# Kernel optimization log

Hardware: AMD Instinct MI355X
Metric: run time of the kernel (lower is better)

Reference implementation:

```python
import jax, jax.numpy as jnp
import numpy as np

N, E, G = 50000, 320000, 256
BN_EPS = 1e-5
HEADS = 4


def _bn(x, g, b):
    # eval-mode BatchNorm1d with running_mean=0, running_var=1
    return g * (x * np.float32(1.0 / np.sqrt(1.0 + BN_EPS))) + b


def _mlp(x, w1, b1, w2, b2):
    return jax.nn.relu(x @ w1 + b1) @ w2 + b2


def _gatv2(x, src, dst, ea, lw, lb, rw, rb, ew, att, bias):
    n = x.shape[0]
    H = HEADS
    C = lw.shape[1] // H
    # self-loops with edge_attr = mean of incoming edge features (fill_value='mean')
    deg = jax.ops.segment_sum(jnp.ones((ea.shape[0],), x.dtype), dst, num_segments=n)
    loop_ea = jax.ops.segment_sum(ea, dst, num_segments=n) / jnp.maximum(deg, 1.0)[:, None]
    ar = jnp.arange(n)
    s = jnp.concatenate([src, ar])
    d = jnp.concatenate([dst, ar])
    ea_all = jnp.concatenate([ea, loop_ea], axis=0)
    xl = (x @ lw + lb).reshape(n, H, C)   # lin_l (source / message features)
    xr = (x @ rw + rb).reshape(n, H, C)   # lin_r (target)
    ee = (ea_all @ ew).reshape(-1, H, C)  # lin_edge (no bias)
    m = jax.nn.leaky_relu(xl[s] + xr[d] + ee, 0.2)       # [E+N, H, C]
    a = jnp.einsum('ehc,hc->eh', m, att)                 # attention logits
    amax = jax.ops.segment_max(a, d, num_segments=n)
    ex = jnp.exp(a - amax[d])
    den = jax.ops.segment_sum(ex, d, num_segments=n)
    w = ex / den[d]                                      # scatter-softmax over target
    out = jax.ops.segment_sum(xl[s] * w[..., None], d, num_segments=n)
    return out.reshape(n, H * C) + bias


def _meta(x, ea, u, src, dst, batch, ep, gp, up):
    # EdgeModel -> NodeModel(GATv2 + relu) -> GlobalModel (residuals=False, eval dropout)
    ea2 = _mlp(jnp.concatenate([x[src], x[dst], ea], axis=1), *ep)
    xn = jax.nn.relu(_gatv2(x, src, dst, ea2, *gp))
    pooled = jax.ops.segment_sum(xn, batch, num_segments=G)
    u2 = _mlp(jnp.concatenate([u, pooled], axis=1), *up)
    return xn, ea2, u2


def _forward(x, edge_attr, e1_w1, e1_b1, e1_w2, e1_b2, g1_lw, g1_lb, g1_rw, g1_rb, g1_ew, g1_att, g1_bias, u1_w1, u1_b1, u1_w2, u1_b2, bn_n_g, bn_n_b, bn_e_g, bn_e_b, bn_u_g, bn_u_b, e2_w1, e2_b1, e2_w2, e2_b2, g2_lw, g2_lb, g2_rw, g2_rb, g2_ew, g2_att, g2_bias, u2_w1, u2_b1, u2_w2, u2_b2, fc1_w, fc1_b, fc2_w, fc2_b, src, dst, batch):
    u0 = jnp.zeros((G, 256), x.dtype)
    x1, ea1, u1 = _meta(x, edge_attr, u0, src, dst, batch,
                        (e1_w1, e1_b1, e1_w2, e1_b2),
                        (g1_lw, g1_lb, g1_rw, g1_rb, g1_ew, g1_att, g1_bias),
                        (u1_w1, u1_b1, u1_w2, u1_b2))
    x1 = _bn(x1, bn_n_g, bn_n_b)
    ea1 = _bn(ea1, bn_e_g, bn_e_b)
    u1 = _bn(u1, bn_u_g, bn_u_b)
    _, _, u2 = _meta(x1, ea1, u1, src, dst, batch,
                     (e2_w1, e2_b1, e2_w2, e2_b2),
                     (g2_lw, g2_lb, g2_rw, g2_rb, g2_ew, g2_att, g2_bias),
                     (u2_w1, u2_b1, u2_w2, u2_b2))
    h = jax.nn.relu(u2 @ fc1_w + fc1_b)
    return h @ fc2_w + fc2_b


def setup_inputs() -> dict:
    key = jax.random.key(0)
    ks = iter(jax.random.split(key, 64))
    rp = lambda shape: jax.random.normal(next(ks), shape, jnp.float32) * 0.05
    inp = {}
    inp['x'] = jax.random.normal(next(ks), (N, 64), jnp.float32)
    inp['edge_attr'] = jax.random.normal(next(ks), (E, 16), jnp.float32)
    # layer 1: EdgeModel(64,16,h=64,out=128), GATv2(64->256,H=4,edge=128), Global(256+256->256)
    inp.update(e1_w1=rp((144, 64)), e1_b1=rp((64,)), e1_w2=rp((64, 128)), e1_b2=rp((128,)))
    inp.update(g1_lw=rp((64, 256)), g1_lb=rp((256,)), g1_rw=rp((64, 256)), g1_rb=rp((256,)),
               g1_ew=rp((128, 256)), g1_att=rp((4, 64)), g1_bias=rp((256,)))
    inp.update(u1_w1=rp((512, 256)), u1_b1=rp((256,)), u1_w2=rp((256, 256)), u1_b2=rp((256,)))
    inp.update(bn_n_g=jnp.ones((256,), jnp.float32), bn_n_b=jnp.zeros((256,), jnp.float32),
               bn_e_g=jnp.ones((128,), jnp.float32), bn_e_b=jnp.zeros((128,), jnp.float32),
               bn_u_g=jnp.ones((256,), jnp.float32), bn_u_b=jnp.zeros((256,), jnp.float32))
    # layer 2: EdgeModel(256,128,h=128,out=128), GATv2(256->256,H=4,edge=128), Global
    inp.update(e2_w1=rp((640, 128)), e2_b1=rp((128,)), e2_w2=rp((128, 128)), e2_b2=rp((128,)))
    inp.update(g2_lw=rp((256, 256)), g2_lb=rp((256,)), g2_rw=rp((256, 256)), g2_rb=rp((256,)),
               g2_ew=rp((128, 256)), g2_att=rp((4, 64)), g2_bias=rp((256,)))
    inp.update(u2_w1=rp((512, 256)), u2_b1=rp((256,)), u2_w2=rp((256, 256)), u2_b2=rp((256,)))
    inp.update(fc1_w=rp((256, 64)), fc1_b=rp((64,)), fc2_w=rp((64, 1)), fc2_b=rp((1,)))
    inp['edge_index'] = jax.random.randint(next(ks), (2, E), 0, N, jnp.int64)
    inp['batch'] = jnp.sort(jax.random.randint(next(ks), (N,), 0, G, jnp.int64))
    return inp


def reference(x, edge_attr, e1_w1, e1_b1, e1_w2, e1_b2, g1_lw, g1_lb, g1_rw, g1_rb, g1_ew, g1_att, g1_bias, u1_w1, u1_b1, u1_w2, u1_b2, bn_n_g, bn_n_b, bn_e_g, bn_e_b, bn_u_g, bn_u_b, e2_w1, e2_b1, e2_w2, e2_b2, g2_lw, g2_lb, g2_rw, g2_rb, g2_ew, g2_att, g2_bias, u2_w1, u2_b1, u2_w2, u2_b2, fc1_w, fc1_b, fc2_w, fc2_b, edge_index, batch):
    return _forward(x, edge_attr, e1_w1, e1_b1, e1_w2, e1_b2, g1_lw, g1_lb, g1_rw, g1_rb, g1_ew, g1_att, g1_bias, u1_w1, u1_b1, u1_w2, u1_b2, bn_n_g, bn_n_b, bn_e_g, bn_e_b, bn_u_g, bn_u_b, e2_w1, e2_b1, e2_w2, e2_b2, g2_lw, g2_lb, g2_rw, g2_rb, g2_ew, g2_att, g2_bias, u2_w1, u2_b1, u2_w2, u2_b2, fc1_w, fc1_b, fc2_w, fc2_b, edge_index[0], edge_index[1], batch)
```

## Files before the change

### kernel.cpp

```cpp
#include <hip/hip_runtime.h>
#include <hip/hip_bf16.h>
#include <hip/hip_fp8.h>
#include <cstdint>
#include <cstddef>

#define INVS 0.99999500003749968f
#define G_GRAPHS 256

using bf16 = __hip_bfloat16;
using short8 = __attribute__((ext_vector_type(8))) short;
using floatx4 = __attribute__((ext_vector_type(4))) float;

__device__ __forceinline__ unsigned short f2bf(float v) {
    union { float f; unsigned u; } x; x.f = v;
    unsigned r = x.u + 0x7fffu + ((x.u >> 16) & 1u);
    return (unsigned short)(r >> 16);
}
__device__ __forceinline__ float bfu(unsigned short u) { return __uint_as_float((unsigned)u << 16); }
__device__ __forceinline__ float bfu_lo(unsigned v) { return __uint_as_float(v << 16); }
__device__ __forceinline__ float bfu_hi(unsigned v) { return __uint_as_float(v & 0xffff0000u); }
__device__ __forceinline__ float fp82f(unsigned char b) {
    __hip_fp8_e4m3 q; q.__x = b; return (float)q;
}
__device__ __forceinline__ unsigned pk_bf16(float a, float b) {
// ... 192 lines not shown
    for (int tt = 0; tt < 2; ++tt) {
        int col = (nq + tt) * 16 + lr;
        float bv = (col >= 64) ? b1[col - 64] : 0.f;
        for (int r = 0; r < 4; ++r)
            Ot[lq * 4 + r][col] = (short)f2bf(acc[tt][r] + bv);
    }
    __syncthreads();
    {
        int r = t >> 4, c = t & 15;
        long long n = n0 + r;
        if (n < N)
            *(short8*)(void*)(pre1 + n * 128 + c * 8) = *(const short8*)&Ot[r][c * 8];
    }
}

__global__ __launch_bounds__(256) void edge_mlp1_mfma_k(
    const bf16* __restrict__ pre1, const float* __restrict__ ea,
    const int* __restrict__ csr_src, const int* __restrict__ csr_dst,
    const int* __restrict__ csr_eid,
    const short* __restrict__ w1c,
    const short* __restrict__ w2s, const float* __restrict__ b2,
    const short* __restrict__ ews,
    unsigned char* __restrict__ ee8, int NT, int E) {
    __shared__ float Ps[32][76];
    __shared__ short Ae[32][40];
    __shared__ short Ht[32][72];
    __shared__ short A2[32][136];
    __shared__ int sdv[32][3];
    unsigned char* Et = (unsigned char*)&Ps[0][0];
    int t = threadIdx.x;
    long long s0 = (long long)blockIdx.x * 32;
    if (t < 96) {
        int r = t & 31, which = t >> 5;
        long long s = s0 + r;
        int v = (which == 2) ? E : 0;
        if (s < NT) v = (which == 0) ? csr_src[s] : (which == 1 ? csr_dst[s] : csr_eid[s]);
        sdv[r][which] = v;
    }
    __syncthreads();
    {
        int r = t >> 3, c = t & 7;
        long long s = s0 + r;
        bool ok = (s < NT) && (sdv[r][2] < E);
        float p[8];
        if (ok) {
            short8 vs = *(const short8*)(const void*)(pre1 + (long long)sdv[r][0] * 128 + c * 8);
// ... 92 lines not shown
        for (int tt = 0; tt < 8; ++tt) {
            int ch0 = (mb + tt) * 16 + lq * 4;
            unsigned u = pk_fp8x4(acc3[tt][0], acc3[tt][1], acc3[tt][2], acc3[tt][3]);
            *(unsigned*)(Et + sl * 272 + ch0) = u;
        }
    }
    __syncthreads();
    for (int i = t; i < 512; i += 256) {
        int r = i >> 4, c = i & 15;
        long long s = s0 + r;
        if (s < NT)
            *(uint4*)(ee8 + s * 256 + c * 16) = *(const uint4*)(Et + r * 272 + c * 16);
    }
}

template <int K, typename T>
__global__ __launch_bounds__(256) void node_linear_mfma_k(
    const T* x, const short* __restrict__ ws,
    const float* __restrict__ bl, const float* __restrict__ br,
    bf16* __restrict__ xl, bf16* xr, int N) {
    __shared__ short At[16][K + 8];
    __shared__ short Ot[16][520];
    int t = threadIdx.x;
    long long n0 = (long long)blockIdx.x * 16;
    if (sizeof(T) == 4) {
        for (int i = t; i < 16 * (K / 4); i += 256) {
            int r = i / (K / 4), c = i % (K / 4);
            long long n = n0 + r;
            float4 v = {0.f, 0.f, 0.f, 0.f};
            if (n < N) v = *(const float4*)((const float*)x + n * K + c * 4);
            ushort4 pk;
            pk.x = f2bf(v.x); pk.y = f2bf(v.y); pk.z = f2bf(v.z); pk.w = f2bf(v.w);
            *(ushort4*)&At[r][c * 4] = pk;
        }
    } else {
        for (int i = t; i < 16 * (K / 8); i += 256) {
            int r = i / (K / 8), c = i % (K / 8);
            long long n = n0 + r;
            short8 v = {0, 0, 0, 0, 0, 0, 0, 0};
            if (n < N) v = *(const short8*)(const void*)((const bf16*)x + n * K + c * 8);
            *(short8*)&At[r][c * 8] = v;
        }
    }
    __syncthreads();

    int w = t >> 6, lane = t & 63;
    int nr = lane & 15, lq = lane >> 4;

    floatx4 acc[8];
    #pragma unroll
    for (int i = 0; i < 8; ++i) acc[i] = (floatx4){0.f, 0.f, 0.f, 0.f};
    for (int kk = 0; kk < K / 32; ++kk) {
        short8 bfr = *(const short8*)&At[nr][kk * 32 + lq * 8];
        #pragma unroll
        for (int tt = 0; tt < 8; ++tt) {
            short8 a = *(const short8*)(ws + ((long long)((kk * 32 + w * 8 + tt) * 64 + lane)) * 8);
            acc[tt] = __builtin_amdgcn_mfma_f32_16x16x32_bf16(a, bfr, acc[tt], 0, 0, 0);
        }
    }
    #pragma unroll
    for (int tt = 0; tt < 8; ++tt) {
        int ch0 = (w * 8 + tt) * 16 + lq * 4;
        const float* bp = (ch0 < 256) ? (bl + ch0) : (br + (ch0 - 256));
        float4 bv = *(const float4*)bp;
        uint2 o;
        o.x = pk_bf16(acc[tt][0] + bv.x, acc[tt][1] + bv.y);
        o.y = pk_bf16(acc[tt][2] + bv.z, acc[tt][3] + bv.w);
        *(uint2*)&Ot[nr][ch0] = o;
    }
    __syncthreads();
    for (int i = t; i < 1024; i += 256) {
        int r = i >> 6, c = i & 63;
        long long n = n0 + r;
        if (n < N) {
            short8 v = *(const short8*)&Ot[r][c * 8];
            if (c < 32) *(short8*)(void*)(xl + n * 256 + c * 8) = v;
            else        *(short8*)(void*)(xr + n * 256 + (c - 32) * 8) = v;
        }
    }
}

__global__ __launch_bounds__(256) void pre_mfma_k(
    const bf16* __restrict__ x, const short* __restrict__ ws,
    const float* __restrict__ bx, bf16* __restrict__ out, int N) {
    __shared__ short At[16][264];
    __shared__ short Ot[16][264];
    int t = threadIdx.x;
    long long n0 = (long long)blockIdx.x * 16;
    for (int i = t; i < 512; i += 256) {
        int r = i >> 5, c = i & 31;
        long long n = n0 + r;
        short8 v = {0, 0, 0, 0, 0, 0, 0, 0};
        if (n < N) v = *(const short8*)(const void*)(x + n * 256 + c * 8);
        *(short8*)&At[r][c * 8] = v;
    }
    __syncthreads();
// ... 15 lines not shown
    #pragma unroll
    for (int tt = 0; tt < 4; ++tt) {
        int ch0 = (w * 4 + tt) * 16 + lq * 4;
        float4 bv = *(const float4*)(bx + ch0);
        uint2 o;
        o.x = pk_bf16(acc[tt][0] + bv.x, acc[tt][1] + bv.y);
        o.y = pk_bf16(acc[tt][2] + bv.z, acc[tt][3] + bv.w);
        *(uint2*)&Ot[nr][ch0] = o;
    }
    __syncthreads();
    for (int i = t; i < 512; i += 256) {
        int r = i >> 5, c = i & 31;
        long long n = n0 + r;
        if (n < N)
            *(short8*)(void*)(out + n * 256 + c * 8) = *(const short8*)&Ot[r][c * 8];
    }
}

template <bool L1>
__global__ __launch_bounds__(256) void gat_fused_k(
    const unsigned char* __restrict__ ee8, const bf16* __restrict__ xl, const bf16* xr,
    const int* __restrict__ off, const int* __restrict__ csr_src,
    const float* __restrict__ att, const float* __restrict__ bias,
    const float* __restrict__ bng, const float* __restrict__ bnb,
    const int* __restrict__ batch,
    bf16* x1bn, float* __restrict__ pooled, int N) {
    __shared__ float ps[4][260];
    __shared__ int bid[4];
    int t = threadIdx.x;
    int w = t >> 6, lane = t & 63;
// ... 154 lines not shown
        int f = g2 >> 6, lane = g2 & 63;
        int kk = f >> 3, tt = f & 7;
        int n = tt * 16 + (lane & 15);
        int k0 = kk * 32 + (lane >> 4) * 8;
        short8 v;
        for (int j = 0; j < 8; ++j) v[j] = (short)f2bf(w2[(k0 + j) * 128 + n]);
        *(short8*)(w2s + (long long)g2 * 8) = v;
    } else if (gid < 12544) {
        int j = gid - 12288;
        b1x[j] = 0.f;
    } else if (gid < 12672) {
        int j = gid - 12544;
        float acc = b1[j];
        for (int c = 0; c < 128; ++c) acc += bb[c] * w1[(512 + c) * 128 + j];
        b1x[128 + j] = acc;
    }
}

__global__ __launch_bounds__(256) void edge_mlp2_mfma_k(
    const bf16* __restrict__ xpre, const bf16* __restrict__ pre1,
    const float* __restrict__ ea,
    const int* __restrict__ csr_src, const int* __restrict__ csr_dst,
    const int* __restrict__ csr_eid,
    const short* __restrict__ w1c, const short* __restrict__ w2s1,
    const float* __restrict__ e1_b2,
    const short* __restrict__ w1s,
    const short* __restrict__ w2s, const float* __restrict__ b2,
    const short* __restrict__ ews,
    unsigned char* __restrict__ ee8, int NT, int E) {
    __shared__ short Zt[32][136];
    __shared__ short Ht[32][136];
    __shared__ short Xt[32][136];
    __shared__ int sdv[32][3];
    unsigned char* Et = (unsigned char*)&Xt[0][0];
    int t = threadIdx.x;
    long long s0 = (long long)blockIdx.x * 32;
    if (t < 96) {
        int r = t & 31, which = t >> 5;
        long long s = s0 + r;
        int v = (which == 2) ? E : 0;
        if (s < NT) v = (which == 0) ? csr_src[s] : (which == 1 ? csr_dst[s] : csr_eid[s]);
        sdv[r][which] = v;
    }
    __syncthreads();
    {
        int r = t >> 3, c = t & 7;
        long long s = s0 + r;
        bool ok = (s < NT) && (sdv[r][2] < E);
        uint4 o = {0, 0, 0, 0};
        if (ok) {
            short8 vs = *(const short8*)(const void*)(pre1 + (long long)sdv[r][0] * 128 + c * 8);
            short8 vd = *(const short8*)(const void*)(pre1 + (long long)sdv[r][1] * 128 + 64 + c * 8);
            float p[8];
            #pragma unroll
            for (int j = 0; j < 8; ++j)
                p[j] = bfu((unsigned short)vs[j]) + bfu((unsigned short)vd[j]);
            o.x = pk_bf16(p[0], p[1]); o.y = pk_bf16(p[2], p[3]);
            o.z = pk_bf16(p[4], p[5]); o.w = pk_bf16(p[6], p[7]);
        }
        *(uint4*)&Zt[r][c * 8] = o;
    }
    if (t < 128) {
        int r = t >> 2, c = t & 3;
        long long s = s0 + r;
        int eid = sdv[r][2];
        float4 v = {0.f, 0.f, 0.f, 0.f};
        if (s < NT && eid < E) v = *(const float4*)(ea + (long long)eid * 16 + c * 4);
        ushort4 pk;
        pk.x = f2bf(v.x); pk.y = f2bf(v.y); pk.z = f2bf(v.z); pk.w = f2bf(v.w);
        *(ushort4*)&Zt[r][96 + c * 4] = pk;
    } else {
        int i = t - 128;
        int r = i >> 2, c = i & 3;
        *(ushort4*)&Zt[r][96 + 16 + c * 4] = (ushort4){0, 0, 0, 0};
    }
    __syncthreads();

    int w = t >> 6, lane = t & 63;
    int sl = (w & 1) * 16 + (lane & 15);
    int lq = lane >> 4;

    {
        int mb = (w >> 1) * 2;
        floatx4 acc[2];
        #pragma unroll
        for (int tt = 0; tt < 2; ++tt) {
            uint2 pv = *(const uint2*)&Zt[sl][(mb + tt) * 16 + lq * 4];
            acc[tt] = (floatx4){bfu_lo(pv.x), bfu_hi(pv.x), bfu_lo(pv.y), bfu_hi(pv.y)};
        }
        short8 bfr = *(const short8*)&Zt[sl][96 + lq * 8];
        #pragma unroll
        for (int tt = 0; tt < 2; ++tt) {
            short8 a = *(const short8*)(w1c + ((long long)((mb + tt) * 64 + lane)) * 8);
            acc[tt] = __builtin_amdgcn_mfma_f32_16x16x32_bf16(a, bfr, acc[tt], 0, 0, 0);
        }
        #pragma unroll
        for (int tt = 0; tt < 2; ++tt) {
            int ch0 = (mb + tt) * 16 + lq * 4;
            uint2 o;
            o.x = pk_bf16(fmaxf(acc[tt][0], 0.f), fmaxf(acc[tt][1], 0.f));
            o.y = pk_bf16(fmaxf(acc[tt][2], 0.f), fmaxf(acc[tt][3], 0.f));
            *(uint2*)&Ht[sl][ch0] = o;
        }
    }
    __syncthreads();

    for (int i = t; i < 512; i += 256) {
        int r = i >> 4, c = i & 15;
        long long s = s0 + r;
        bool ok = (s < NT) && (sdv[r][2] < E);
        uint4 o = {0, 0, 0, 0};
        if (ok) {
            short8 vs = *(const short8*)(const void*)(xpre + (long long)sdv[r][0] * 256 + c * 8);
            short8 vd = *(const short8*)(const void*)(xpre + (long long)sdv[r][1] * 256 + 128 + c * 8);
            float p[8];
            #pragma unroll
            for (int j = 0; j < 8; ++j)
                p[j] = bfu((unsigned short)vs[j]) + bfu((unsigned short)vd[j]);
            o.x = pk_bf16(p[0], p[1]); o.y = pk_bf16(p[2], p[3]);
            o.z = pk_bf16(p[4], p[5]); o.w = pk_bf16(p[6], p[7]);
        }
        *(uint4*)&Xt[r][c * 8] = o;
    }
    {
        int mb = (w >> 1) * 4;
        floatx4 acc2[4];
        #pragma unroll
        for (int i = 0; i < 4; ++i) acc2[i] = (floatx4){0.f, 0.f, 0.f, 0.f};
        #pragma unroll
        for (int kk = 0; kk < 2; ++kk) {
            short8 bfr = *(const short8*)&Ht[sl][kk * 32 + lq * 8];
            #pragma unroll
            for (int tt = 0; tt < 4; ++tt) {
                short8 a = *(const short8*)(w2s1 + ((long long)((kk * 8 + mb + tt) * 64 + lane)) * 8);
                acc2[tt] = __builtin_amdgcn_mfma_f32_16x16x32_bf16(a, bfr, acc2[tt], 0, 0, 0);
            }
        }
        #pragma unroll
        for (int tt = 0; tt < 4; ++tt) {
            int ch0 = (mb + tt) * 16 + lq * 4;
            float4 bv = *(const float4*)(e1_b2 + ch0);
            uint2 o;
            o.x = pk_bf16(acc2[tt][0] + bv.x, acc2[tt][1] + bv.y);
            o.y = pk_bf16(acc2[tt][2] + bv.z, acc2[tt][3] + bv.w);
            *(uint2*)&Zt[sl][ch0] = o;
        }
    }
    __syncthreads();

    {
        int mb = (w >> 1) * 4;
        floatx4 acc[4];
        #pragma unroll
        for (int tt = 0; tt < 4; ++tt) {
            uint2 pv = *(const uint2*)&Xt[sl][(mb + tt) * 16 + lq * 4];
            acc[tt] = (floatx4){bfu_lo(pv.x), bfu_hi(pv.x), bfu_lo(pv.y), bfu_hi(pv.y)};
        }
        #pragma unroll
        for (int kk = 0; kk < 4; ++kk) {
            short8 bfr = *(const short8*)&Zt[sl][kk * 32 + lq * 8];
            #pragma unroll
            for (int tt = 0; tt < 4; ++tt) {
                short8 a = *(const short8*)(w1s + ((long long)(((16 + kk) * 8 + mb + tt) * 64 + lane)) * 8);
                acc[tt] = __builtin_amdgcn_mfma_f32_16x16x32_bf16(a, bfr, acc[tt], 0, 0, 0);
            }
        }
        #pragma unroll
        for (int tt = 0; tt < 4; ++tt) {
            int ch0 = (mb + tt) * 16 + lq * 4;
            uint2 o;
            o.x = pk_bf16(fmaxf(acc[tt][0], 0.f), fmaxf(acc[tt][1], 0.f));
            o.y = pk_bf16(fmaxf(acc[tt][2], 0.f), fmaxf(acc[tt][3], 0.f));
            *(uint2*)&Ht[sl][ch0] = o;
        }
    }
    __syncthreads();

    {
        int mb = (w >> 1) * 4;
        floatx4 acc2[4];
        #pragma unroll
        for (int i = 0; i < 4; ++i) acc2[i] = (floatx4){0.f, 0.f, 0.f, 0.f};
        #pragma unroll
        for (int kk = 0; kk < 4; ++kk) {
            short8 bfr = *(const short8*)&Ht[sl][kk * 32 + lq * 8];
            #pragma unroll
            for (int tt = 0; tt < 4; ++tt) {
                short8 a = *(const short8*)(w2s + ((long long)((kk * 8 + mb + tt) * 64 + lane)) * 8);
                acc2[tt] = __builtin_amdgcn_mfma_f32_16x16x32_bf16(a, bfr, acc2[tt], 0, 0, 0);
            }
        }
        #pragma unroll
        for (int tt = 0; tt < 4; ++tt) {
            int ch0 = (mb + tt) * 16 + lq * 4;
            float4 bv = *(const float4*)(b2 + ch0);
            uint2 o;
            o.x = pk_bf16(acc2[tt][0] + bv.x, acc2[tt][1] + bv.y);
            o.y = pk_bf16(acc2[tt][2] + bv.z, acc2[tt][3] + bv.w);
            *(uint2*)&Zt[sl][ch0] = o;
        }
    }
    __syncthreads();

    {
        int mb = (w >> 1) * 8;
        floatx4 acc3[8];
        #pragma unroll
        for (int i = 0; i < 8; ++i) acc3[i] = (floatx4){0.f, 0.f, 0.f, 0.f};
        #pragma unroll
        for (int kk = 0; kk < 4; ++kk) {
            short8 bfr = *(const short8*)&Zt[sl][kk * 32 + lq * 8];
            #pragma unroll
            for (int tt = 0; tt < 8; ++tt) {
                short8 a = *(const short8*)(ews + ((long long)((kk * 16 + mb + tt) * 64 + lane)) * 8);
                acc3[tt] = __builtin_amdgcn_mfma_f32_16x16x32_bf16(a, bfr, acc3[tt], 0, 0, 0);
            }
        }
        #pragma unroll
        for (int tt = 0; tt < 8; ++tt) {
            int ch0 = (mb + tt) * 16 + lq * 4;
            unsigned u = pk_fp8x4(acc3[tt][0], acc3[tt][1], acc3[tt][2], acc3[tt][3]);
            *(unsigned*)(Et + sl * 272 + ch0) = u;
        }
    }
    __syncthreads();
    for (int i = t; i < 512; i += 256) {
        int r = i >> 4, c = i & 15;
        long long s = s0 + r;
        if (s < NT && sdv[r][2] < E)
            *(uint4*)(ee8 + s * 256 + c * 16) = *(const uint4*)(Et + r * 272 + c * 16);
    }
}

__global__ void final_mlp_k(const float* __restrict__ u1bn, const float* __restrict__ pooled,
                            const float* __restrict__ w1, const float* __restrict__ b1,
                            const float* __restrict__ w2, const float* __restrict__ b2,
                            const float* __restrict__ f1w, const float* __restrict__ f1b,
                            const float* __restrict__ f2w, const float* __restrict__ f2b,
                            float* __restrict__ out) {
    __shared__ float ub[256], pb[256], h[256], u2[256];
    int t = threadIdx.x, g = blockIdx.x;
    ub[t] = u1bn[g * 256 + t];
    pb[t] = pooled[g * 256 + t];
    __syncthreads();
    float acc = b1[t];
// ... 58 lines not shown
    const float* u2_b2 = (const float*)d_in[37];
    const float* fc1_w = (const float*)d_in[38];
    const float* fc1_b = (const float*)d_in[39];
    const float* fc2_w = (const float*)d_in[40];
    const float* fc2_b = (const float*)d_in[41];
    const int* edge_index = (const int*)d_in[42];
    const int* batch = (const int*)d_in[43];

    const int N = in_sizes[0] / 64;
    const int E = in_sizes[1] / 16;
    const int NT = E + N;
    const int G = G_GRAPHS;
    const int* src = edge_index;
    const int* dst = edge_index + E;
    const int NB = (NT + 31) / 32;
    const int NSB = (N + 2047) / 2048;

    char* p = (char*)d_ws;
    auto alloc = [&](size_t bytes) { char* r = p; p += (bytes + 255) & ~(size_t)255; return r; };
    bf16* xl    = (bf16*)alloc((size_t)N * 256 * 2);
    bf16* xr    = (bf16*)alloc((size_t)N * 256 * 2);
    bf16* x1bn  = xr;
    unsigned char* ee8 = (unsigned char*)alloc((size_t)NT * 256);
    bf16* pre1  = (bf16*)alloc((size_t)N * 128 * 2);
    int* degi   = (int*)alloc((size_t)N * 4);
    int* off    = (int*)alloc((size_t)(N + 1) * 4);
    int* fillc  = (int*)alloc((size_t)N * 4);
    int* csr_src = (int*)alloc((size_t)NT * 4);
    int* csr_dst = (int*)alloc((size_t)NT * 4);
    int* csr_eid = (int*)alloc((size_t)NT * 4);
    int* bsum   = (int*)alloc((size_t)(NSB + 1) * 4);
    int* boff   = (int*)alloc((size_t)(NSB + 1) * 4);
    float* pooled = (float*)alloc((size_t)G * 256 * 4);
    float* u1bn = (float*)alloc((size_t)G * 256 * 4);
    short* w1s  = (short*)alloc((size_t)20 * 8 * 64 * 8 * 2);
    short* w2s  = (short*)alloc((size_t)4 * 8 * 64 * 8 * 2);
    float* b1x  = (float*)alloc((size_t)256 * 4);
// ... 11 lines not shown
    hipMemsetAsync(pooled, 0, (size_t)G * 256 * 4, stream);
    degi_k<<<(E + 255) / 256, 256, 0, stream>>>(dst, degi, E);
    scan_blk_k<<<NSB, 1024, 0, stream>>>(degi, off, bsum, N);
    scan_top_k<<<1, 64, 0, stream>>>(bsum, boff, off, NSB, N);
    scan_add_k<<<(N + 255) / 256, 256, 0, stream>>>(off, boff, N);
    fill_csr_k<<<(max(E, N) + 255) / 256, 256, 0, stream>>>(src, dst, off, fillc,
                                                            csr_src, csr_dst, csr_eid, E, N);

    conv_weights1_k<<<9, 256, 0, stream>>>(e1_w1, e1_w2, w1p, w1c, w2s1);
    conv_ew_k<<<16, 256, 0, stream>>>(g1_ew, ews1);
    conv_ew_k<<<16, 256, 0, stream>>>(g2_ew, ews2);
    conv_nodew_k<64><<<16, 256, 0, stream>>>(g1_lw, g1_rw, nw1);
    conv_nodew_k<256><<<64, 256, 0, stream>>>(g2_lw, g2_rw, nw2);
    conv_pre2w_k<<<32, 256, 0, stream>>>(e2_w1, nwp);
    pre1_mfma_k<<<(N + 15) / 16, 256, 0, stream>>>(x, w1p, e1_b1, pre1, N);
    edge_mlp1_mfma_k<<<NB, 256, 0, stream>>>(pre1, edge_attr, csr_src, csr_dst, csr_eid,
                                             w1c, w2s1, e1_b2, ews1, ee8, NT, E);
    node_linear_mfma_k<64, float><<<(N + 15) / 16, 256, 0, stream>>>(x, nw1, g1_lb, g1_rb, xl, xr, N);
    gat_fused_k<true><<<(N + 3) / 4, 256, 0, stream>>>(ee8, xl, xr, off, csr_src,
                                                       g1_att, g1_bias, bn_n_g, bn_n_b,
                                                       batch, x1bn, pooled, N);
    global_mlp1_k<<<G, 256, 0, stream>>>(pooled, u1_w1, u1_b1, u1_w2, u1_b2, bn_u_g, bn_u_b, u1bn);

    conv_weights_k<<<50, 256, 0, stream>>>(e2_w1, e2_w2, e2_b1, bn_e_g, bn_e_b, w1s, w2s, b1x);
    pre_mfma_k<<<(N + 15) / 16, 256, 0, stream>>>(x1bn, nwp, b1x, xl, N);
    edge_mlp2_mfma_k<<<NB, 256, 0, stream>>>(xl, pre1, edge_attr, csr_src, csr_dst, csr_eid,
                                             w1c, w2s1, e1_b2, w1s, w2s, e2_b2, ews2,
                                             ee8, NT, E);
    node_linear_mfma_k<256, bf16><<<(N + 15) / 16, 256, 0, stream>>>(x1bn, nw2, g2_lb, g2_rb, xl, xr, N);
    hipMemsetAsync(pooled, 0, (size_t)G * 256 * 4, stream);
    gat_fused_k<false><<<(N + 3) / 4, 256, 0, stream>>>(ee8, xl, xr, off, csr_src,
                                                        g2_att, g2_bias, nullptr, nullptr,
                                                        batch, nullptr, pooled, N);
    final_mlp_k<<<G, 256, 0, stream>>>(u1bn, pooled, u2_w1, u2_b1, u2_w2, u2_b2,
                                       fc1_w, fc1_b, fc2_w, fc2_b, (float*)d_out);
}
```

Measured before the change: 695.4 us.

## Merge node-linear GEMMs into edge-MLP kernels as extra blocks of one launch

The node lin_l/lin_r projection and the edge MLP now run as one kernel launch per layer. The first NLB blocks do the node projection and the remaining blocks do the edge MLP, with both paths sharing one raw shared-memory buffer. Layer 2 gets separate xl2/xr2 buffers so the node projection no longer overwrites xl, which the edge MLP still reads as its precomputed input. This removes a launch and its serialization and lets the two independent workloads overlap on the GPU. In exchange it costs extra workspace memory, and the shared-memory size is set by the larger path, which may lower occupancy.

```diff
diff --git a/kernel.cpp b/kernel.cpp
--- a/kernel.cpp
+++ b/kernel.cpp
@@ -230,7 +230,10 @@
     }
 }
 
-__global__ __launch_bounds__(256) void edge_mlp1_mfma_k(
+__global__ __launch_bounds__(256) void fused_l1_k(
+    const float* __restrict__ x, const short* __restrict__ nw,
+    const float* __restrict__ bl, const float* __restrict__ br,
+    bf16* __restrict__ xl, bf16* __restrict__ xr, int N, int NLB,
     const bf16* __restrict__ pre1, const float* __restrict__ ea,
     const int* __restrict__ csr_src, const int* __restrict__ csr_dst,
     const int* __restrict__ csr_eid,
@@ -238,14 +241,64 @@
     const short* __restrict__ w2s, const float* __restrict__ b2,
     const short* __restrict__ ews,
     unsigned char* __restrict__ ee8, int NT, int E) {
-    __shared__ float Ps[32][76];
-    __shared__ short Ae[32][40];
-    __shared__ short Ht[32][72];
-    __shared__ short A2[32][136];
-    __shared__ int sdv[32][3];
-    unsigned char* Et = (unsigned char*)&Ps[0][0];
+    __shared__ __align__(16) char smem[25984];
     int t = threadIdx.x;
-    long long s0 = (long long)blockIdx.x * 32;
+    if ((int)blockIdx.x < NLB) {
+        short (*At)[72]  = (short(*)[72])smem;
+        short (*Ot)[520] = (short(*)[520])(smem + 2304);
+        long long n0 = (long long)blockIdx.x * 16;
+        {
+            int r = t >> 4, c = t & 15;
+            long long n = n0 + r;
+            float4 v = {0.f, 0.f, 0.f, 0.f};
+            if (n < N) v = *(const float4*)(x + n * 64 + c * 4);
+            ushort4 pk;
+            pk.x = f2bf(v.x); pk.y = f2bf(v.y); pk.z = f2bf(v.z); pk.w = f2bf(v.w);
+            *(ushort4*)&At[r][c * 4] = pk;
+        }
+        __syncthreads();
+        int w = t >> 6, lane = t & 63;
+        int nr = lane & 15, lq = lane >> 4;
+        floatx4 acc[8];
+        #pragma unroll
+        for (int i = 0; i < 8; ++i) acc[i] = (floatx4){0.f, 0.f, 0.f, 0.f};
+        for (int kk = 0; kk < 2; ++kk) {
+            short8 bfr = *(const short8*)&At[nr][kk * 32 + lq * 8];
+            #pragma unroll
+            for (int tt = 0; tt < 8; ++tt) {
+                short8 a = *(const short8*)(nw + ((long long)((kk * 32 + w * 8 + tt) * 64 + lane)) * 8);
+                acc[tt] = __builtin_amdgcn_mfma_f32_16x16x32_bf16(a, bfr, acc[tt], 0, 0, 0);
+            }
+        }
+        #pragma unroll
+        for (int tt = 0; tt < 8; ++tt) {
+            int ch0 = (w * 8 + tt) * 16 + lq * 4;
+            const float* bp = (ch0 < 256) ? (bl + ch0) : (br + (ch0 - 256));
+            float4 bv = *(const float4*)bp;
+            uint2 o;
+            o.x = pk_bf16(acc[tt][0] + bv.x, acc[tt][1] + bv.y);
+            o.y = pk_bf16(acc[tt][2] + bv.z, acc[tt][3] + bv.w);
+            *(uint2*)&Ot[nr][ch0] = o;
+        }
+        __syncthreads();
+        for (int i = t; i < 1024; i += 256) {
+            int r = i >> 6, c = i & 63;
+            long long n = n0 + r;
+            if (n < N) {
+                short8 v = *(const short8*)&Ot[r][c * 8];
+                if (c < 32) *(short8*)(void*)(xl + n * 256 + c * 8) = v;
+                else        *(short8*)(void*)(xr + n * 256 + (c - 32) * 8) = v;
+            }
+        }
+        return;
+    }
+    float (*Ps)[76]  = (float(*)[76])smem;
+    short (*Ae)[40]  = (short(*)[40])(smem + 9728);
+    short (*Ht)[72]  = (short(*)[72])(smem + 12288);
+    short (*A2)[136] = (short(*)[136])(smem + 16896);
+    int (*sdv)[3]    = (int(*)[3])(smem + 25600);
+    unsigned char* Et = (unsigned char*)smem;
+    long long s0 = (long long)(blockIdx.x - NLB) * 32;
     if (t < 96) {
         int r = t & 31, which = t >> 5;
         long long s = s0 + r;
@@ -368,72 +421,6 @@
     }
 }
 
-template <int K, typename T>
-__global__ __launch_bounds__(256) void node_linear_mfma_k(
-    const T* x, const short* __restrict__ ws,
-    const float* __restrict__ bl, const float* __restrict__ br,
-    bf16* __restrict__ xl, bf16* xr, int N) {
-    __shared__ short At[16][K + 8];
-    __shared__ short Ot[16][520];
-    int t = threadIdx.x;
-    long long n0 = (long long)blockIdx.x * 16;
-    if (sizeof(T) == 4) {
-        for (int i = t; i < 16 * (K / 4); i += 256) {
-            int r = i / (K / 4), c = i % (K / 4);
-            long long n = n0 + r;
-            float4 v = {0.f, 0.f, 0.f, 0.f};
-            if (n < N) v = *(const float4*)((const float*)x + n * K + c * 4);
-            ushort4 pk;
-            pk.x = f2bf(v.x); pk.y = f2bf(v.y); pk.z = f2bf(v.z); pk.w = f2bf(v.w);
-            *(ushort4*)&At[r][c * 4] = pk;
-        }
-    } else {
-        for (int i = t; i < 16 * (K / 8); i += 256) {
-            int r = i / (K / 8), c = i % (K / 8);
-            long long n = n0 + r;
-            short8 v = {0, 0, 0, 0, 0, 0, 0, 0};
-            if (n < N) v = *(const short8*)(const void*)((const bf16*)x + n * K + c * 8);
-            *(short8*)&At[r][c * 8] = v;
-        }
-    }
-    __syncthreads();
-
-    int w = t >> 6, lane = t & 63;
-    int nr = lane & 15, lq = lane >> 4;
-
-    floatx4 acc[8];
-    #pragma unroll
-    for (int i = 0; i < 8; ++i) acc[i] = (floatx4){0.f, 0.f, 0.f, 0.f};
-    for (int kk = 0; kk < K / 32; ++kk) {
-        short8 bfr = *(const short8*)&At[nr][kk * 32 + lq * 8];
-        #pragma unroll
-        for (int tt = 0; tt < 8; ++tt) {
-            short8 a = *(const short8*)(ws + ((long long)((kk * 32 + w * 8 + tt) * 64 + lane)) * 8);
-            acc[tt] = __builtin_amdgcn_mfma_f32_16x16x32_bf16(a, bfr, acc[tt], 0, 0, 0);
-        }
-    }
-    #pragma unroll
-    for (int tt = 0; tt < 8; ++tt) {
-        int ch0 = (w * 8 + tt) * 16 + lq * 4;
-        const float* bp = (ch0 < 256) ? (bl + ch0) : (br + (ch0 - 256));
-        float4 bv = *(const float4*)bp;
-        uint2 o;
-        o.x = pk_bf16(acc[tt][0] + bv.x, acc[tt][1] + bv.y);
-        o.y = pk_bf16(acc[tt][2] + bv.z, acc[tt][3] + bv.w);
-        *(uint2*)&Ot[nr][ch0] = o;
-    }
-    __syncthreads();
-    for (int i = t; i < 1024; i += 256) {
-        int r = i >> 6, c = i & 63;
-        long long n = n0 + r;
-        if (n < N) {
-            short8 v = *(const short8*)&Ot[r][c * 8];
-            if (c < 32) *(short8*)(void*)(xl + n * 256 + c * 8) = v;
-            else        *(short8*)(void*)(xr + n * 256 + (c - 32) * 8) = v;
-        }
-    }
-}
-
 __global__ __launch_bounds__(256) void pre_mfma_k(
     const bf16* __restrict__ x, const short* __restrict__ ws,
     const float* __restrict__ bx, bf16* __restrict__ out, int N) {
@@ -479,6 +466,272 @@
         long long n = n0 + r;
         if (n < N)
             *(short8*)(void*)(out + n * 256 + c * 8) = *(const short8*)&Ot[r][c * 8];
+    }
+}
+
+__global__ __launch_bounds__(256) void fused_l2_k(
+    const bf16* __restrict__ xin, const short* __restrict__ nw,
+    const float* __restrict__ bl, const float* __restrict__ br,
+    bf16* __restrict__ xl2, bf16* __restrict__ xr2, int N, int NLB,
+    const bf16* __restrict__ xpre, const bf16* __restrict__ pre1,
+    const float* __restrict__ ea,
+    const int* __restrict__ csr_src, const int* __restrict__ csr_dst,
+    const int* __restrict__ csr_eid,
+    const short* __restrict__ w1c, const short* __restrict__ w2s1,
+    const float* __restrict__ e1_b2,
+    const short* __restrict__ w1s,
+    const short* __restrict__ w2s, const float* __restrict__ b2,
+    const short* __restrict__ ews,
+    unsigned char* __restrict__ ee8, int NT, int E) {
+    __shared__ __align__(16) char smem[26496];
+    int t = threadIdx.x;
+    if ((int)blockIdx.x < NLB) {
+        short (*At)[264] = (short(*)[264])smem;
+        short (*Ot)[520] = (short(*)[520])(smem + 8448);
+        long long n0 = (long long)blockIdx.x * 16;
+        for (int i = t; i < 512; i += 256) {
+            int r = i >> 5, c = i & 31;
+            long long n = n0 + r;
+            short8 v = {0, 0, 0, 0, 0, 0, 0, 0};
+            if (n < N) v = *(const short8*)(const void*)(xin + n * 256 + c * 8);
+            *(short8*)&At[r][c * 8] = v;
+        }
+        __syncthreads();
+        int w = t >> 6, lane = t & 63;
+        int nr = lane & 15, lq = lane >> 4;
+        floatx4 acc[8];
+        #pragma unroll
+        for (int i = 0; i < 8; ++i) acc[i] = (floatx4){0.f, 0.f, 0.f, 0.f};
+        for (int kk = 0; kk < 8; ++kk) {
+            short8 bfr = *(const short8*)&At[nr][kk * 32 + lq * 8];
+            #pragma unroll
+            for (int tt = 0; tt < 8; ++tt) {
+                short8 a = *(const short8*)(nw + ((long long)((kk * 32 + w * 8 + tt) * 64 + lane)) * 8);
+                acc[tt] = __builtin_amdgcn_mfma_f32_16x16x32_bf16(a, bfr, acc[tt], 0, 0, 0);
+            }
+        }
+        #pragma unroll
+        for (int tt = 0; tt < 8; ++tt) {
+            int ch0 = (w * 8 + tt) * 16 + lq * 4;
+            const float* bp = (ch0 < 256) ? (bl + ch0) : (br + (ch0 - 256));
+            float4 bv = *(const float4*)bp;
+            uint2 o;
+            o.x = pk_bf16(acc[tt][0] + bv.x, acc[tt][1] + bv.y);
+            o.y = pk_bf16(acc[tt][2] + bv.z, acc[tt][3] + bv.w);
+            *(uint2*)&Ot[nr][ch0] = o;
+        }
+        __syncthreads();
+        for (int i = t; i < 1024; i += 256) {
+            int r = i >> 6, c = i & 63;
+            long long n = n0 + r;
+            if (n < N) {
+                short8 v = *(const short8*)&Ot[r][c * 8];
+                if (c < 32) *(short8*)(void*)(xl2 + n * 256 + c * 8) = v;
+                else        *(short8*)(void*)(xr2 + n * 256 + (c - 32) * 8) = v;
+            }
+        }
+        return;
+    }
+    short (*Zt)[136] = (short(*)[136])smem;
+    short (*Ht)[136] = (short(*)[136])(smem + 8704);
+    short (*Xt)[136] = (short(*)[136])(smem + 17408);
+    int (*sdv)[3]    = (int(*)[3])(smem + 26112);
+    unsigned char* Et = (unsigned char*)(smem + 17408);
+    long long s0 = (long long)(blockIdx.x - NLB) * 32;
+    if (t < 96) {
+        int r = t & 31, which = t >> 5;
+        long long s = s0 + r;
+        int v = (which == 2) ? E : 0;
+        if (s < NT) v = (which == 0) ? csr_src[s] : (which == 1 ? csr_dst[s] : csr_eid[s]);
+        sdv[r][which] = v;
+    }
+    __syncthreads();
+    {
+        int r = t >> 3, c = t & 7;
+        long long s = s0 + r;
+        bool ok = (s < NT) && (sdv[r][2] < E);
+        uint4 o = {0, 0, 0, 0};
+        if (ok) {
+            short8 vs = *(const short8*)(const void*)(pre1 + (long long)sdv[r][0] * 128 + c * 8);
+            short8 vd = *(const short8*)(const void*)(pre1 + (long long)sdv[r][1] * 128 + 64 + c * 8);
+            float p[8];
+            #pragma unroll
+            for (int j = 0; j < 8; ++j)
+                p[j] = bfu((unsigned short)vs[j]) + bfu((unsigned short)vd[j]);
+            o.x = pk_bf16(p[0], p[1]); o.y = pk_bf16(p[2], p[3]);
+            o.z = pk_bf16(p[4], p[5]); o.w = pk_bf16(p[6], p[7]);
+        }
+        *(uint4*)&Zt[r][c * 8] = o;
+    }
+    if (t < 128) {
+        int r = t >> 2, c = t & 3;
+        long long s = s0 + r;
+        int eid = sdv[r][2];
+        float4 v = {0.f, 0.f, 0.f, 0.f};
+        if (s < NT && eid < E) v = *(const float4*)(ea + (long long)eid * 16 + c * 4);
+        ushort4 pk;
+        pk.x = f2bf(v.x); pk.y = f2bf(v.y); pk.z = f2bf(v.z); pk.w = f2bf(v.w);
+        *(ushort4*)&Zt[r][96 + c * 4] = pk;
+    } else {
+        int i = t - 128;
+        int r = i >> 2, c = i & 3;
+        *(ushort4*)&Zt[r][96 + 16 + c * 4] = (ushort4){0, 0, 0, 0};
+    }
+    __syncthreads();
+
+    int w = t >> 6, lane = t & 63;
+    int sl = (w & 1) * 16 + (lane & 15);
+    int lq = lane >> 4;
+
+    {
+        int mb = (w >> 1) * 2;
+        floatx4 acc[2];
+        #pragma unroll
+        for (int tt = 0; tt < 2; ++tt) {
+            uint2 pv = *(const uint2*)&Zt[sl][(mb + tt) * 16 + lq * 4];
+            acc[tt] = (floatx4){bfu_lo(pv.x), bfu_hi(pv.x), bfu_lo(pv.y), bfu_hi(pv.y)};
+        }
+        short8 bfr = *(const short8*)&Zt[sl][96 + lq * 8];
+        #pragma unroll
+        for (int tt = 0; tt < 2; ++tt) {
+            short8 a = *(const short8*)(w1c + ((long long)((mb + tt) * 64 + lane)) * 8);
+            acc[tt] = __builtin_amdgcn_mfma_f32_16x16x32_bf16(a, bfr, acc[tt], 0, 0, 0);
+        }
+        #pragma unroll
+        for (int tt = 0; tt < 2; ++tt) {
+            int ch0 = (mb + tt) * 16 + lq * 4;
+            uint2 o;
+            o.x = pk_bf16(fmaxf(acc[tt][0], 0.f), fmaxf(acc[tt][1], 0.f));
+            o.y = pk_bf16(fmaxf(acc[tt][2], 0.f), fmaxf(acc[tt][3], 0.f));
+            *(uint2*)&Ht[sl][ch0] = o;
+        }
+    }
+    __syncthreads();
+
+    for (int i = t; i < 512; i += 256) {
+        int r = i >> 4, c = i & 15;
+        long long s = s0 + r;
+        bool ok = (s < NT) && (sdv[r][2] < E);
+        uint4 o = {0, 0, 0, 0};
+        if (ok) {
+            short8 vs = *(const short8*)(const void*)(xpre + (long long)sdv[r][0] * 256 + c * 8);
+            short8 vd = *(const short8*)(const void*)(xpre + (long long)sdv[r][1] * 256 + 128 + c * 8);
+            float p[8];
+            #pragma unroll
+            for (int j = 0; j < 8; ++j)
+                p[j] = bfu((unsigned short)vs[j]) + bfu((unsigned short)vd[j]);
+            o.x = pk_bf16(p[0], p[1]); o.y = pk_bf16(p[2], p[3]);
+            o.z = pk_bf16(p[4], p[5]); o.w = pk_bf16(p[6], p[7]);
+        }
+        *(uint4*)&Xt[r][c * 8] = o;
+    }
+    {
+        int mb = (w >> 1) * 4;
+        floatx4 acc2[4];
+        #pragma unroll
+        for (int i = 0; i < 4; ++i) acc2[i] = (floatx4){0.f, 0.f, 0.f, 0.f};
+        #pragma unroll
+        for (int kk = 0; kk < 2; ++kk) {
+            short8 bfr = *(const short8*)&Ht[sl][kk * 32 + lq * 8];
+            #pragma unroll
+            for (int tt = 0; tt < 4; ++tt) {
+                short8 a = *(const short8*)(w2s1 + ((long long)((kk * 8 + mb + tt) * 64 + lane)) * 8);
+                acc2[tt] = __builtin_amdgcn_mfma_f32_16x16x32_bf16(a, bfr, acc2[tt], 0, 0, 0);
+            }
+        }
+        #pragma unroll
+        for (int tt = 0; tt < 4; ++tt) {
+            int ch0 = (mb + tt) * 16 + lq * 4;
+            float4 bv = *(const float4*)(e1_b2 + ch0);
+            uint2 o;
+            o.x = pk_bf16(acc2[tt][0] + bv.x, acc2[tt][1] + bv.y);
+            o.y = pk_bf16(acc2[tt][2] + bv.z, acc2[tt][3] + bv.w);
+            *(uint2*)&Zt[sl][ch0] = o;
+        }
+    }
+    __syncthreads();
+
+    {
+        int mb = (w >> 1) * 4;
+        floatx4 acc[4];
+        #pragma unroll
+        for (int tt = 0; tt < 4; ++tt) {
+            uint2 pv = *(const uint2*)&Xt[sl][(mb + tt) * 16 + lq * 4];
+            acc[tt] = (floatx4){bfu_lo(pv.x), bfu_hi(pv.x), bfu_lo(pv.y), bfu_hi(pv.y)};
+        }
+        #pragma unroll
+        for (int kk = 0; kk < 4; ++kk) {
+            short8 bfr = *(const short8*)&Zt[sl][kk * 32 + lq * 8];
+            #pragma unroll
+            for (int tt = 0; tt < 4; ++tt) {
+                short8 a = *(const short8*)(w1s + ((long long)(((16 + kk) * 8 + mb + tt) * 64 + lane)) * 8);
+                acc[tt] = __builtin_amdgcn_mfma_f32_16x16x32_bf16(a, bfr, acc[tt], 0, 0, 0);
+            }
+        }
+        #pragma unroll
+        for (int tt = 0; tt < 4; ++tt) {
+            int ch0 = (mb + tt) * 16 + lq * 4;
+            uint2 o;
+            o.x = pk_bf16(fmaxf(acc[tt][0], 0.f), fmaxf(acc[tt][1], 0.f));
+            o.y = pk_bf16(fmaxf(acc[tt][2], 0.f), fmaxf(acc[tt][3], 0.f));
+            *(uint2*)&Ht[sl][ch0] = o;
+        }
+    }
+    __syncthreads();
+
+    {
+        int mb = (w >> 1) * 4;
+        floatx4 acc2[4];
+        #pragma unroll
+        for (int i = 0; i < 4; ++i) acc2[i] = (floatx4){0.f, 0.f, 0.f, 0.f};
+        #pragma unroll
+        for (int kk = 0; kk < 4; ++kk) {
+            short8 bfr = *(const short8*)&Ht[sl][kk * 32 + lq * 8];
+            #pragma unroll
+            for (int tt = 0; tt < 4; ++tt) {
+                short8 a = *(const short8*)(w2s + ((long long)((kk * 8 + mb + tt) * 64 + lane)) * 8);
+                acc2[tt] = __builtin_amdgcn_mfma_f32_16x16x32_bf16(a, bfr, acc2[tt], 0, 0, 0);
+            }
+        }
+        #pragma unroll
+        for (int tt = 0; tt < 4; ++tt) {
+            int ch0 = (mb + tt) * 16 + lq * 4;
+            float4 bv = *(const float4*)(b2 + ch0);
+            uint2 o;
+            o.x = pk_bf16(acc2[tt][0] + bv.x, acc2[tt][1] + bv.y);
+            o.y = pk_bf16(acc2[tt][2] + bv.z, acc2[tt][3] + bv.w);
+            *(uint2*)&Zt[sl][ch0] = o;
+        }
+    }
+    __syncthreads();
+
+    {
+        int mb = (w >> 1) * 8;
+        floatx4 acc3[8];
+        #pragma unroll
+        for (int i = 0; i < 8; ++i) acc3[i] = (floatx4){0.f, 0.f, 0.f, 0.f};
+        #pragma unroll
+        for (int kk = 0; kk < 4; ++kk) {
+            short8 bfr = *(const short8*)&Zt[sl][kk * 32 + lq * 8];
+            #pragma unroll
+            for (int tt = 0; tt < 8; ++tt) {
+                short8 a = *(const short8*)(ews + ((long long)((kk * 16 + mb + tt) * 64 + lane)) * 8);
+                acc3[tt] = __builtin_amdgcn_mfma_f32_16x16x32_bf16(a, bfr, acc3[tt], 0, 0, 0);
+            }
+        }
+        #pragma unroll
+        for (int tt = 0; tt < 8; ++tt) {
+            int ch0 = (mb + tt) * 16 + lq * 4;
+            unsigned u = pk_fp8x4(acc3[tt][0], acc3[tt][1], acc3[tt][2], acc3[tt][3]);
+            *(unsigned*)(Et + sl * 272 + ch0) = u;
+        }
+    }
+    __syncthreads();
+    for (int i = t; i < 512; i += 256) {
+        int r = i >> 4, c = i & 15;
+        long long s = s0 + r;
+        if (s < NT && sdv[r][2] < E)
+            *(uint4*)(ee8 + s * 256 + c * 16) = *(const uint4*)(Et + r * 272 + c * 16);
     }
 }
 
@@ -663,221 +916,6 @@
         float acc = b1[j];
         for (int c = 0; c < 128; ++c) acc += bb[c] * w1[(512 + c) * 128 + j];
         b1x[128 + j] = acc;
-    }
-}
-
-__global__ __launch_bounds__(256) void edge_mlp2_mfma_k(
-    const bf16* __restrict__ xpre, const bf16* __restrict__ pre1,
-    const float* __restrict__ ea,
-    const int* __restrict__ csr_src, const int* __restrict__ csr_dst,
-    const int* __restrict__ csr_eid,
-    const short* __restrict__ w1c, const short* __restrict__ w2s1,
-    const float* __restrict__ e1_b2,
-    const short* __restrict__ w1s,
-    const short* __restrict__ w2s, const float* __restrict__ b2,
-    const short* __restrict__ ews,
-    unsigned char* __restrict__ ee8, int NT, int E) {
-    __shared__ short Zt[32][136];
-    __shared__ short Ht[32][136];
-    __shared__ short Xt[32][136];
-    __shared__ int sdv[32][3];
-    unsigned char* Et = (unsigned char*)&Xt[0][0];
-    int t = threadIdx.x;
-    long long s0 = (long long)blockIdx.x * 32;
-    if (t < 96) {
-        int r = t & 31, which = t >> 5;
-        long long s = s0 + r;
-        int v = (which == 2) ? E : 0;
-        if (s < NT) v = (which == 0) ? csr_src[s] : (which == 1 ? csr_dst[s] : csr_eid[s]);
-        sdv[r][which] = v;
-    }
-    __syncthreads();
-    {
-        int r = t >> 3, c = t & 7;
-        long long s = s0 + r;
-        bool ok = (s < NT) && (sdv[r][2] < E);
-        uint4 o = {0, 0, 0, 0};
-        if (ok) {
-            short8 vs = *(const short8*)(const void*)(pre1 + (long long)sdv[r][0] * 128 + c * 8);
-            short8 vd = *(const short8*)(const void*)(pre1 + (long long)sdv[r][1] * 128 + 64 + c * 8);
-            float p[8];
-            #pragma unroll
-            for (int j = 0; j < 8; ++j)
-                p[j] = bfu((unsigned short)vs[j]) + bfu((unsigned short)vd[j]);
-            o.x = pk_bf16(p[0], p[1]); o.y = pk_bf16(p[2], p[3]);
-            o.z = pk_bf16(p[4], p[5]); o.w = pk_bf16(p[6], p[7]);
-        }
-        *(uint4*)&Zt[r][c * 8] = o;
-    }
-    if (t < 128) {
-        int r = t >> 2, c = t & 3;
-        long long s = s0 + r;
-        int eid = sdv[r][2];
-        float4 v = {0.f, 0.f, 0.f, 0.f};
-        if (s < NT && eid < E) v = *(const float4*)(ea + (long long)eid * 16 + c * 4);
-        ushort4 pk;
-        pk.x = f2bf(v.x); pk.y = f2bf(v.y); pk.z = f2bf(v.z); pk.w = f2bf(v.w);
-        *(ushort4*)&Zt[r][96 + c * 4] = pk;
-    } else {
-        int i = t - 128;
-        int r = i >> 2, c = i & 3;
-        *(ushort4*)&Zt[r][96 + 16 + c * 4] = (ushort4){0, 0, 0, 0};
-    }
-    __syncthreads();
-
-    int w = t >> 6, lane = t & 63;
-    int sl = (w & 1) * 16 + (lane & 15);
-    int lq = lane >> 4;
-
-    {
-        int mb = (w >> 1) * 2;
-        floatx4 acc[2];
-        #pragma unroll
-        for (int tt = 0; tt < 2; ++tt) {
-            uint2 pv = *(const uint2*)&Zt[sl][(mb + tt) * 16 + lq * 4];
-            acc[tt] = (floatx4){bfu_lo(pv.x), bfu_hi(pv.x), bfu_lo(pv.y), bfu_hi(pv.y)};
-        }
-        short8 bfr = *(const short8*)&Zt[sl][96 + lq * 8];
-        #pragma unroll
-        for (int tt = 0; tt < 2; ++tt) {
-            short8 a = *(const short8*)(w1c + ((long long)((mb + tt) * 64 + lane)) * 8);
-            acc[tt] = __builtin_amdgcn_mfma_f32_16x16x32_bf16(a, bfr, acc[tt], 0, 0, 0);
-        }
-        #pragma unroll
-        for (int tt = 0; tt < 2; ++tt) {
-            int ch0 = (mb + tt) * 16 + lq * 4;
-            uint2 o;
-            o.x = pk_bf16(fmaxf(acc[tt][0], 0.f), fmaxf(acc[tt][1], 0.f));
-            o.y = pk_bf16(fmaxf(acc[tt][2], 0.f), fmaxf(acc[tt][3], 0.f));
-            *(uint2*)&Ht[sl][ch0] = o;
-        }
-    }
-    __syncthreads();
-
-    for (int i = t; i < 512; i += 256) {
-        int r = i >> 4, c = i & 15;
-        long long s = s0 + r;
-        bool ok = (s < NT) && (sdv[r][2] < E);
-        uint4 o = {0, 0, 0, 0};
-        if (ok) {
-            short8 vs = *(const short8*)(const void*)(xpre + (long long)sdv[r][0] * 256 + c * 8);
-            short8 vd = *(const short8*)(const void*)(xpre + (long long)sdv[r][1] * 256 + 128 + c * 8);
-            float p[8];
-            #pragma unroll
-            for (int j = 0; j < 8; ++j)
-                p[j] = bfu((unsigned short)vs[j]) + bfu((unsigned short)vd[j]);
-            o.x = pk_bf16(p[0], p[1]); o.y = pk_bf16(p[2], p[3]);
-            o.z = pk_bf16(p[4], p[5]); o.w = pk_bf16(p[6], p[7]);
-        }
-        *(uint4*)&Xt[r][c * 8] = o;
-    }
-    {
-        int mb = (w >> 1) * 4;
-        floatx4 acc2[4];
-        #pragma unroll
-        for (int i = 0; i < 4; ++i) acc2[i] = (floatx4){0.f, 0.f, 0.f, 0.f};
-        #pragma unroll
-        for (int kk = 0; kk < 2; ++kk) {
-            short8 bfr = *(const short8*)&Ht[sl][kk * 32 + lq * 8];
-            #pragma unroll
-            for (int tt = 0; tt < 4; ++tt) {
-                short8 a = *(const short8*)(w2s1 + ((long long)((kk * 8 + mb + tt) * 64 + lane)) * 8);
-                acc2[tt] = __builtin_amdgcn_mfma_f32_16x16x32_bf16(a, bfr, acc2[tt], 0, 0, 0);
-            }
-        }
-        #pragma unroll
-        for (int tt = 0; tt < 4; ++tt) {
-            int ch0 = (mb + tt) * 16 + lq * 4;
-            float4 bv = *(const float4*)(e1_b2 + ch0);
-            uint2 o;
-            o.x = pk_bf16(acc2[tt][0] + bv.x, acc2[tt][1] + bv.y);
-            o.y = pk_bf16(acc2[tt][2] + bv.z, acc2[tt][3] + bv.w);
-            *(uint2*)&Zt[sl][ch0] = o;
-        }
-    }
-    __syncthreads();
-
-    {
-        int mb = (w >> 1) * 4;
-        floatx4 acc[4];
-        #pragma unroll
-        for (int tt = 0; tt < 4; ++tt) {
-            uint2 pv = *(const uint2*)&Xt[sl][(mb + tt) * 16 + lq * 4];
-            acc[tt] = (floatx4){bfu_lo(pv.x), bfu_hi(pv.x), bfu_lo(pv.y), bfu_hi(pv.y)};
-        }
-        #pragma unroll
-        for (int kk = 0; kk < 4; ++kk) {
-            short8 bfr = *(const short8*)&Zt[sl][kk * 32 + lq * 8];
-            #pragma unroll
-            for (int tt = 0; tt < 4; ++tt) {
-                short8 a = *(const short8*)(w1s + ((long long)(((16 + kk) * 8 + mb + tt) * 64 + lane)) * 8);
-                acc[tt] = __builtin_amdgcn_mfma_f32_16x16x32_bf16(a, bfr, acc[tt], 0, 0, 0);
-            }
-        }
-        #pragma unroll
-        for (int tt = 0; tt < 4; ++tt) {
-            int ch0 = (mb + tt) * 16 + lq * 4;
-            uint2 o;
-            o.x = pk_bf16(fmaxf(acc[tt][0], 0.f), fmaxf(acc[tt][1], 0.f));
-            o.y = pk_bf16(fmaxf(acc[tt][2], 0.f), fmaxf(acc[tt][3], 0.f));
-            *(uint2*)&Ht[sl][ch0] = o;
-        }
-    }
-    __syncthreads();
-
-    {
-        int mb = (w >> 1) * 4;
-        floatx4 acc2[4];
-        #pragma unroll
-        for (int i = 0; i < 4; ++i) acc2[i] = (floatx4){0.f, 0.f, 0.f, 0.f};
-        #pragma unroll
-        for (int kk = 0; kk < 4; ++kk) {
-            short8 bfr = *(const short8*)&Ht[sl][kk * 32 + lq * 8];
-            #pragma unroll
-            for (int tt = 0; tt < 4; ++tt) {
-                short8 a = *(const short8*)(w2s + ((long long)((kk * 8 + mb + tt) * 64 + lane)) * 8);
-                acc2[tt] = __builtin_amdgcn_mfma_f32_16x16x32_bf16(a, bfr, acc2[tt], 0, 0, 0);
-            }
-        }
-        #pragma unroll
-        for (int tt = 0; tt < 4; ++tt) {
-            int ch0 = (mb + tt) * 16 + lq * 4;
-            float4 bv = *(const float4*)(b2 + ch0);
-            uint2 o;
-            o.x = pk_bf16(acc2[tt][0] + bv.x, acc2[tt][1] + bv.y);
-            o.y = pk_bf16(acc2[tt][2] + bv.z, acc2[tt][3] + bv.w);
-            *(uint2*)&Zt[sl][ch0] = o;
-        }
-    }
-    __syncthreads();
-
-    {
-        int mb = (w >> 1) * 8;
-        floatx4 acc3[8];
-        #pragma unroll
-        for (int i = 0; i < 8; ++i) acc3[i] = (floatx4){0.f, 0.f, 0.f, 0.f};
-        #pragma unroll
-        for (int kk = 0; kk < 4; ++kk) {
-            short8 bfr = *(const short8*)&Zt[sl][kk * 32 + lq * 8];
-            #pragma unroll
-            for (int tt = 0; tt < 8; ++tt) {
-                short8 a = *(const short8*)(ews + ((long long)((kk * 16 + mb + tt) * 64 + lane)) * 8);
-                acc3[tt] = __builtin_amdgcn_mfma_f32_16x16x32_bf16(a, bfr, acc3[tt], 0, 0, 0);
-            }
-        }
-        #pragma unroll
-        for (int tt = 0; tt < 8; ++tt) {
-            int ch0 = (mb + tt) * 16 + lq * 4;
-            unsigned u = pk_fp8x4(acc3[tt][0], acc3[tt][1], acc3[tt][2], acc3[tt][3]);
-            *(unsigned*)(Et + sl * 272 + ch0) = u;
-        }
-    }
-    __syncthreads();
-    for (int i = t; i < 512; i += 256) {
-        int r = i >> 4, c = i & 15;
-        long long s = s0 + r;
-        if (s < NT && sdv[r][2] < E)
-            *(uint4*)(ee8 + s * 256 + c * 16) = *(const uint4*)(Et + r * 272 + c * 16);
     }
 }
 
@@ -966,6 +1004,7 @@
     const int* src = edge_index;
     const int* dst = edge_index + E;
     const int NB = (NT + 31) / 32;
+    const int NLB = (N + 15) / 16;
     const int NSB = (N + 2047) / 2048;
 
     char* p = (char*)d_ws;
@@ -973,6 +1012,8 @@
     bf16* xl    = (bf16*)alloc((size_t)N * 256 * 2);
     bf16* xr    = (bf16*)alloc((size_t)N * 256 * 2);
     bf16* x1bn  = xr;
+    bf16* xl2   = (bf16*)alloc((size_t)N * 256 * 2);
+    bf16* xr2   = (bf16*)alloc((size_t)N * 256 * 2);
     unsigned char* ee8 = (unsigned char*)alloc((size_t)NT * 256);
     bf16* pre1  = (bf16*)alloc((size_t)N * 128 * 2);
     int* degi   = (int*)alloc((size_t)N * 4);
@@ -1014,9 +1055,9 @@
     conv_nodew_k<256><<<64, 256, 0, stream>>>(g2_lw, g2_rw, nw2);
     conv_pre2w_k<<<32, 256, 0, stream>>>(e2_w1, nwp);
     pre1_mfma_k<<<(N + 15) / 16, 256, 0, stream>>>(x, w1p, e1_b1, pre1, N);
-    edge_mlp1_mfma_k<<<NB, 256, 0, stream>>>(pre1, edge_attr, csr_src, csr_dst, csr_eid,
+    fused_l1_k<<<NLB + NB, 256, 0, stream>>>(x, nw1, g1_lb, g1_rb, xl, xr, N, NLB,
+                                             pre1, edge_attr, csr_src, csr_dst, csr_eid,
                                              w1c, w2s1, e1_b2, ews1, ee8, NT, E);
-    node_linear_mfma_k<64, float><<<(N + 15) / 16, 256, 0, stream>>>(x, nw1, g1_lb, g1_rb, xl, xr, N);
     gat_fused_k<true><<<(N + 3) / 4, 256, 0, stream>>>(ee8, xl, xr, off, csr_src,
                                                        g1_att, g1_bias, bn_n_g, bn_n_b,
                                                        batch, x1bn, pooled, N);
@@ -1024,12 +1065,12 @@
 
     conv_weights_k<<<50, 256, 0, stream>>>(e2_w1, e2_w2, e2_b1, bn_e_g, bn_e_b, w1s, w2s, b1x);
     pre_mfma_k<<<(N + 15) / 16, 256, 0, stream>>>(x1bn, nwp, b1x, xl, N);
-    edge_mlp2_mfma_k<<<NB, 256, 0, stream>>>(xl, pre1, edge_attr, csr_src, csr_dst, csr_eid,
+    fused_l2_k<<<NLB + NB, 256, 0, stream>>>(x1bn, nw2, g2_lb, g2_rb, xl2, xr2, N, NLB,
+                                             xl, pre1, edge_attr, csr_src, csr_dst, csr_eid,
                                              w1c, w2s1, e1_b2, w1s, w2s, e2_b2, ews2,
                                              ee8, NT, E);
-    node_linear_mfma_k<256, bf16><<<(N + 15) / 16, 256, 0, stream>>>(x1bn, nw2, g2_lb, g2_rb, xl, xr, N);
     hipMemsetAsync(pooled, 0, (size_t)G * 256 * 4, stream);
-    gat_fused_k<false><<<(N + 3) / 4, 256, 0, stream>>>(ee8, xl, xr, off, csr_src,
+    gat_fused_k<false><<<(N + 3) / 4, 256, 0, stream>>>(ee8, xl2, xr2, off, csr_src,
                                                         g2_att, g2_bias, nullptr, nullptr,
                                                         batch, nullptr, pooled, N);
     final_mlp_k<<<G, 256, 0, stream>>>(u1bn, pooled, u2_w1, u2_b1, u2_w2, u2_b2,
```

New measurement: 700.4 us. No clear change (+0.7%).
